# Optimization experiments

Hardware: AMD Instinct MI355X
Metric: run time of the kernel (lower is better)

## Reference

```python
import jax, jax.numpy as jnp
import numpy as np

RC = 6.0  # cosine cutoff radius

def _cut_fn(r):
    # Behler cosine cutoff: 0.5*(cos(pi*r/rc)+1) for r < rc, else 0
    return jnp.where(r < RC, 0.5 * (jnp.cos(jnp.pi * r / RC) + 1.0), 0.0)

def setup_inputs() -> dict:
    key = jax.random.key(0)
    ks = jax.random.split(key, 6)
    B, N, T, E, Z = 4, 256, 512, 16, 4
    def dist(k):
        return jax.random.uniform(k, (B, N, T), dtype=jnp.float32) * 5.0 + 0.5
    r_ij = dist(ks[0])
    r_ik = dist(ks[1])
    r_jk = dist(ks[2])
    # binary triple mask (float, as multiplied in the original forward)
    mask_triples = (jax.random.uniform(ks[3], (B, N, T)) > 0.3).astype(jnp.float32)
    etas = jax.random.uniform(ks[4], (E,), dtype=jnp.float32) + 0.5
    zetas = jnp.array([1.0, 2.0, 4.0, 8.0], dtype=jnp.float32)
    return {"r_ij": r_ij, "r_ik": r_ik, "r_jk": r_jk,
            "mask_triples": mask_triples, "etas": etas, "zetas": zetas}

def reference(r_ij, r_ik, r_jk, mask_triples, etas, zetas):
    # r_ij, r_ik, r_jk, mask_triples: (B, N, T); etas: (E,); zetas: (Z,)
    r2 = r_ij ** 2 + r_ik ** 2 + r_jk ** 2                       # (B,N,T)
    cut = _cut_fn(r_ij) * _cut_fn(r_ik) * _cut_fn(r_jk)          # (B,N,T)
    radius_part = jnp.exp(-r2[..., None] * etas) * cut[..., None]  # (B,N,T,E)
    cos_theta = r2 / (2.0 * r_ij * r_ik)                          # (B,N,T)
    cos_theta = jnp.where(mask_triples == 0, 0.0, cos_theta)
    base = (1.0 - cos_theta)[..., None] ** zetas                  # (B,N,T,Z)
    angular_part = jnp.concatenate(
        [2.0 ** (1.0 - zetas) * base, 2.0 ** (1.0 + zetas) * base], axis=-1
    )                                                             # (B,N,T,2Z)
    # fused masked outer-product + sum over triples dim (dim 2 in the original)
    f = jnp.einsum('bnt,bnte,bntz->bnez', mask_triples, radius_part, angular_part)
    B, N = r_ij.shape[:2]
    return f.reshape(B, N, -1)                                    # (B,N,E*2Z)
```

## Files before the change

### kernel.cpp

```cpp
#include <hip/hip_runtime.h>
#include <math.h>


#define T_TRIP 512
#define E_N 16

__global__ __launch_bounds__(512, 8) void behler_g2_kernel(
    const float* __restrict__ r_ij, const float* __restrict__ r_ik,
    const float* __restrict__ r_jk, const float* __restrict__ mask,
    const float* __restrict__ etas, const float* __restrict__ zetas,
    float* __restrict__ out)
{
    __shared__ float  R2[T_TRIP];
    __shared__ float4 P[T_TRIP];
    __shared__ float  red[8][E_N][4];

    const int blk = blockIdx.x;
    const int tid = threadIdx.x;
    const size_t idx = (size_t)blk * T_TRIP + tid;

    const float z0 = zetas[0], z1 = zetas[1], z2 = zetas[2], z3 = zetas[3];
    const bool fastz = (z0 == 1.0f && z1 == 2.0f && z2 == 4.0f && z3 == 8.0f);
    const float PI_OVER_RC = 0.52359877559829887f;

    {
        float a = r_ij[idx];
        float b = r_ik[idx];
        float c = r_jk[idx];
        float m = mask[idx];
        float r2 = fmaf(a, a, fmaf(b, b, c * c));
        float fa  = (a < 6.0f) ? 0.5f * (__cosf(a * PI_OVER_RC) + 1.0f) : 0.0f;
        float fb  = (b < 6.0f) ? 0.5f * (__cosf(b * PI_OVER_RC) + 1.0f) : 0.0f;
        float fcv = (c < 6.0f) ? 0.5f * (__cosf(c * PI_OVER_RC) + 1.0f) : 0.0f;
        float w = m * fa * fb * fcv;
        float ct = __fdividef(r2, 2.0f * a * b);
        float4 p;
        if (fastz) {
            float bs = 1.0f - ct;
            float s2 = bs * bs, s4 = s2 * s2, s8 = s4 * s4;
            p = make_float4(w * bs, w * s2, w * s4, w * s8);
        } else {
            if (m == 0.0f) ct = 0.0f;
            float bs = 1.0f - ct;
            p = make_float4(w * powf(bs, z0), w * powf(bs, z1),
                            w * powf(bs, z2), w * powf(bs, z3));
        }
        R2[tid] = r2;
        P[tid] = p;
    }
    __syncthreads();

    const int g = tid >> 4;
    const int e = tid & 15;
    const float me = -etas[e];

    float acc0 = 0.0f, acc1 = 0.0f, acc2 = 0.0f, acc3 = 0.0f;
    #pragma unroll
    for (int i = 0; i < T_TRIP / 32; ++i) {
        int t = (i << 5) + g;
        float x = __expf(R2[t] * me);
        float4 p = P[t];
        acc0 = fmaf(x, p.x, acc0);
        acc1 = fmaf(x, p.y, acc1);
        acc2 = fmaf(x, p.z, acc2);
        acc3 = fmaf(x, p.w, acc3);
    }

    acc0 += __shfl_down(acc0, 32); acc0 += __shfl_down(acc0, 16);
    acc1 += __shfl_down(acc1, 32); acc1 += __shfl_down(acc1, 16);
    acc2 += __shfl_down(acc2, 32); acc2 += __shfl_down(acc2, 16);
    acc3 += __shfl_down(acc3, 32); acc3 += __shfl_down(acc3, 16);

    const int wave = tid >> 6;
    if ((tid & 63) < 16) {
        red[wave][e][0] = acc0;
        red[wave][e][1] = acc1;
        red[wave][e][2] = acc2;
        red[wave][e][3] = acc3;
    }
    __syncthreads();

    if (tid < 128) {
        int ee = tid >> 3, z = tid & 7, j = z & 3;
        float s = 0.0f;
        #pragma unroll
        for (int wv = 0; wv < 8; ++wv) s += red[wv][ee][j];
        float zj = zetas[j];
        float coef = exp2f((z < 4) ? (1.0f - zj) : (1.0f + zj));
        out[(size_t)blk * 128 + tid] = coef * s;
    }
}

extern "C" void kernel_launch(void* const* d_in, const int* in_sizes, int n_in,
                              void* d_out, int out_size, void* d_ws, size_t ws_size,
                              hipStream_t stream) {
    const float* r_ij = (const float*)d_in[0];
    const float* r_ik = (const float*)d_in[1];
    const float* r_jk = (const float*)d_in[2];
    const float* mask = (const float*)d_in[3];
    const float* etas = (const float*)d_in[4];
    const float* zetas = (const float*)d_in[5];
    float* out = (float*)d_out;

    int nblk = out_size / 128;
    behler_g2_kernel<<<nblk, 512, 0, stream>>>(r_ij, r_ik, r_jk, mask,
                                               etas, zetas, out);
}
```

Measured before the change: 9.804 us.

## Process four rows per block to amortize block overhead and batch loads

Each block now handles four (b,n) rows instead of one. It loads all four rows' inputs up front, stages their per-triple terms in larger shared arrays, and reduces each row in turn. This cuts the block count by four and increases outstanding loads per thread. In exchange there are fewer blocks than before, so each CU has fewer waves to hide latency, and shared memory per block grows.

```diff
diff --git a/kernel.cpp b/kernel.cpp
--- a/kernel.cpp
+++ b/kernel.cpp
@@ -3,6 +3,7 @@
 
 
 #define T_TRIP 512
+#define ROWS 4
 #define E_N 16
 
 __global__ __launch_bounds__(512, 8) void behler_g2_kernel(
@@ -11,83 +12,91 @@
     const float* __restrict__ etas, const float* __restrict__ zetas,
     float* __restrict__ out)
 {
-    __shared__ float  R2[T_TRIP];
-    __shared__ float4 P[T_TRIP];
-    __shared__ float  red[8][E_N][4];
+    __shared__ float  R2s[ROWS][T_TRIP];
+    __shared__ float4 Ps[ROWS][T_TRIP];
+    __shared__ float  red[ROWS][8][E_N][4];
 
     const int blk = blockIdx.x;
     const int tid = threadIdx.x;
-    const size_t idx = (size_t)blk * T_TRIP + tid;
+    const size_t row0 = (size_t)blk * ROWS;
 
     const float z0 = zetas[0], z1 = zetas[1], z2 = zetas[2], z3 = zetas[3];
     const bool fastz = (z0 == 1.0f && z1 == 2.0f && z2 == 4.0f && z3 == 8.0f);
     const float PI_OVER_RC = 0.52359877559829887f;
 
-    {
-        float a = r_ij[idx];
-        float b = r_ik[idx];
-        float c = r_jk[idx];
-        float m = mask[idx];
-        float r2 = fmaf(a, a, fmaf(b, b, c * c));
-        float fa  = (a < 6.0f) ? 0.5f * (__cosf(a * PI_OVER_RC) + 1.0f) : 0.0f;
-        float fb  = (b < 6.0f) ? 0.5f * (__cosf(b * PI_OVER_RC) + 1.0f) : 0.0f;
-        float fcv = (c < 6.0f) ? 0.5f * (__cosf(c * PI_OVER_RC) + 1.0f) : 0.0f;
-        float w = m * fa * fb * fcv;
-        float ct = __fdividef(r2, 2.0f * a * b);
+    float a[ROWS], b[ROWS], c[ROWS], m[ROWS];
+    #pragma unroll
+    for (int q = 0; q < ROWS; ++q) {
+        size_t idx = (row0 + q) * T_TRIP + tid;
+        a[q] = r_ij[idx];
+        b[q] = r_ik[idx];
+        c[q] = r_jk[idx];
+        m[q] = mask[idx];
+    }
+    #pragma unroll
+    for (int q = 0; q < ROWS; ++q) {
+        float r2 = fmaf(a[q], a[q], fmaf(b[q], b[q], c[q] * c[q]));
+        float fa  = (a[q] < 6.0f) ? 0.5f * (__cosf(a[q] * PI_OVER_RC) + 1.0f) : 0.0f;
+        float fb  = (b[q] < 6.0f) ? 0.5f * (__cosf(b[q] * PI_OVER_RC) + 1.0f) : 0.0f;
+        float fcv = (c[q] < 6.0f) ? 0.5f * (__cosf(c[q] * PI_OVER_RC) + 1.0f) : 0.0f;
+        float w = m[q] * fa * fb * fcv;
+        float ct = __fdividef(r2, 2.0f * a[q] * b[q]);
         float4 p;
         if (fastz) {
             float bs = 1.0f - ct;
             float s2 = bs * bs, s4 = s2 * s2, s8 = s4 * s4;
             p = make_float4(w * bs, w * s2, w * s4, w * s8);
         } else {
-            if (m == 0.0f) ct = 0.0f;
+            if (m[q] == 0.0f) ct = 0.0f;
             float bs = 1.0f - ct;
             p = make_float4(w * powf(bs, z0), w * powf(bs, z1),
                             w * powf(bs, z2), w * powf(bs, z3));
         }
-        R2[tid] = r2;
-        P[tid] = p;
+        R2s[q][tid] = r2;
+        Ps[q][tid] = p;
     }
     __syncthreads();
 
     const int g = tid >> 4;
     const int e = tid & 15;
     const float me = -etas[e];
+    const int wave = tid >> 6;
 
-    float acc0 = 0.0f, acc1 = 0.0f, acc2 = 0.0f, acc3 = 0.0f;
     #pragma unroll
-    for (int i = 0; i < T_TRIP / 32; ++i) {
-        int t = (i << 5) + g;
-        float x = __expf(R2[t] * me);
-        float4 p = P[t];
-        acc0 = fmaf(x, p.x, acc0);
-        acc1 = fmaf(x, p.y, acc1);
-        acc2 = fmaf(x, p.z, acc2);
-        acc3 = fmaf(x, p.w, acc3);
-    }
-
-    acc0 += __shfl_down(acc0, 32); acc0 += __shfl_down(acc0, 16);
-    acc1 += __shfl_down(acc1, 32); acc1 += __shfl_down(acc1, 16);
-    acc2 += __shfl_down(acc2, 32); acc2 += __shfl_down(acc2, 16);
-    acc3 += __shfl_down(acc3, 32); acc3 += __shfl_down(acc3, 16);
-
-    const int wave = tid >> 6;
-    if ((tid & 63) < 16) {
-        red[wave][e][0] = acc0;
-        red[wave][e][1] = acc1;
-        red[wave][e][2] = acc2;
-        red[wave][e][3] = acc3;
+    for (int q = 0; q < ROWS; ++q) {
+        float acc0 = 0.0f, acc1 = 0.0f, acc2 = 0.0f, acc3 = 0.0f;
+        #pragma unroll
+        for (int i = 0; i < T_TRIP / 32; ++i) {
+            int t = (i << 5) + g;
+            float x = __expf(R2s[q][t] * me);
+            float4 p = Ps[q][t];
+            acc0 = fmaf(x, p.x, acc0);
+            acc1 = fmaf(x, p.y, acc1);
+            acc2 = fmaf(x, p.z, acc2);
+            acc3 = fmaf(x, p.w, acc3);
+        }
+        acc0 += __shfl_down(acc0, 32); acc0 += __shfl_down(acc0, 16);
+        acc1 += __shfl_down(acc1, 32); acc1 += __shfl_down(acc1, 16);
+        acc2 += __shfl_down(acc2, 32); acc2 += __shfl_down(acc2, 16);
+        acc3 += __shfl_down(acc3, 32); acc3 += __shfl_down(acc3, 16);
+        if ((tid & 63) < 16) {
+            red[q][wave][e][0] = acc0;
+            red[q][wave][e][1] = acc1;
+            red[q][wave][e][2] = acc2;
+            red[q][wave][e][3] = acc3;
+        }
     }
     __syncthreads();
 
-    if (tid < 128) {
-        int ee = tid >> 3, z = tid & 7, j = z & 3;
+    {
+        int q = tid >> 7, r = tid & 127;
+        int ee = r >> 3, z = r & 7, j = z & 3;
         float s = 0.0f;
         #pragma unroll
-        for (int wv = 0; wv < 8; ++wv) s += red[wv][ee][j];
+        for (int wv = 0; wv < 8; ++wv) s += red[q][wv][ee][j];
         float zj = zetas[j];
         float coef = exp2f((z < 4) ? (1.0f - zj) : (1.0f + zj));
-        out[(size_t)blk * 128 + tid] = coef * s;
+        out[(row0 + q) * 128 + r] = coef * s;
     }
 }
 
@@ -102,7 +111,7 @@
     const float* zetas = (const float*)d_in[5];
     float* out = (float*)d_out;
 
-    int nblk = out_size / 128;
+    int nblk = out_size / (128 * ROWS);
     behler_g2_kernel<<<nblk, 512, 0, stream>>>(r_ij, r_ik, r_jk, mask,
                                                etas, zetas, out);
 }
```

After: 9.976 us. About the same (+1.8%).
